# Kernel tuning notes

Hardware: AMD Instinct MI355X
Metric: run time of the kernel (lower is better)

## Reference

```python
import jax, jax.numpy as jnp
import numpy as np

D_MODEL = 768
N_HEADS = 12
HEAD_DIM = D_MODEL // N_HEADS


def setup_inputs() -> dict:
    key = jax.random.key(0)
    ks = jax.random.split(key, 9)
    B, S = 2, 2048
    x = jax.random.normal(ks[0], (B, S, D_MODEL), dtype=jnp.float32)
    s = 1.0 / np.sqrt(D_MODEL)
    Wq = jax.random.normal(ks[1], (D_MODEL, D_MODEL), dtype=jnp.float32) * s
    bq = jax.random.normal(ks[2], (D_MODEL,), dtype=jnp.float32) * 0.01
    Wk = jax.random.normal(ks[3], (D_MODEL, D_MODEL), dtype=jnp.float32) * s
    bk = jax.random.normal(ks[4], (D_MODEL,), dtype=jnp.float32) * 0.01
    Wv = jax.random.normal(ks[5], (D_MODEL, D_MODEL), dtype=jnp.float32) * s
    bv = jax.random.normal(ks[6], (D_MODEL,), dtype=jnp.float32) * 0.01
    Wo = jax.random.normal(ks[7], (D_MODEL, D_MODEL), dtype=jnp.float32) * s
    bo = jax.random.normal(ks[8], (D_MODEL,), dtype=jnp.float32) * 0.01
    return {"x": x, "Wq": Wq, "bq": bq, "Wk": Wk, "bk": bk,
            "Wv": Wv, "bv": bv, "Wo": Wo, "bo": bo}


def reference(x, Wq, bq, Wk, bk, Wv, bv, Wo, bo):
    B, S, _ = x.shape
    H, Dh = N_HEADS, HEAD_DIM
    # Projections (torch Linear: x @ W.T + b; here W stored as [in, out])
    q = (x @ Wq + bq).reshape(B, S, H, Dh)
    k = (x @ Wk + bk).reshape(B, S, H, Dh)
    v = (x @ Wv + bv).reshape(B, S, H, Dh)
    scale = 1.0 / jnp.sqrt(jnp.float32(Dh))
    # NOTE: source applies no causal mask despite the class name.
    scores = jnp.einsum('bqhd,bkhd->bhqk', q, k) * scale
    attn = jax.nn.softmax(scores, axis=-1)
    out = jnp.einsum('bhqk,bkhd->bqhd', attn, v).reshape(B, S, H * Dh)
    return out @ Wo + bo
```

## Files before the change

kernel.cpp:

```cpp
#include <hip/hip_runtime.h>

typedef unsigned short u16;
typedef __fp16 halfx8 __attribute__((ext_vector_type(8)));
typedef float floatx4 __attribute__((ext_vector_type(4)));
typedef unsigned short u16x4 __attribute__((ext_vector_type(4)));

#define D_MODEL 768
#define NH 12
#define DH 64
#define SEQ 2048
#define BATCH 2
#define MTOK 4096
#define DQKV 2304

__device__ __forceinline__ u16 f2h(float f) {
    __fp16 h = (__fp16)f;
    return __builtin_bit_cast(u16, h);
}

__device__ __forceinline__ void gload_lds16(const void* g, void* l) {
    __builtin_amdgcn_global_load_lds(
        (const __attribute__((address_space(1))) void*)g,
        (__attribute__((address_space(3))) void*)l, 16, 0, 0);
}


__global__ __launch_bounds__(256) void cvt_x_kernel(const float* __restrict__ x, u16* __restrict__ xh) {
    int i = (blockIdx.x * 256 + threadIdx.x) * 4;
    float4 v = *(const float4*)(x + i);
    u16x4 p;
    p[0] = f2h(v.x); p[1] = f2h(v.y); p[2] = f2h(v.z); p[3] = f2h(v.w);
    *(u16x4*)(xh + i) = p;
}

__global__ __launch_bounds__(256) void concat_bias_kernel(const float* __restrict__ bq, const float* __restrict__ bk,
                                                          const float* __restrict__ bv, float* __restrict__ bqkv) {
    int i = blockIdx.x * 256 + threadIdx.x;
    float v = (i < 768) ? bq[i] : (i < 1536) ? bk[i - 768] : bv[i - 1536];
    bqkv[i] = v;
}

__global__ __launch_bounds__(256) void transpose_w_kernel(const float* __restrict__ Wq, const float* __restrict__ Wk,
                                                          const float* __restrict__ Wv, const float* __restrict__ Wo,
                                                          u16* __restrict__ WqkvT, u16* __restrict__ WoT) {
    int z = blockIdx.z;
    const float* W = (z == 0) ? Wq : (z == 1) ? Wk : (z == 2) ? Wv : Wo;
    u16* dst = (z < 3) ? (WqkvT + (size_t)z * 768 * 768) : WoT;
    int k0 = blockIdx.x * 64, n0 = blockIdx.y * 64;
    __shared__ u16 t[64][72];
    int tid = threadIdx.x;
#pragma unroll
    for (int p = 0; p < 16; ++p) {
        int idx = p * 256 + tid;
        int kr = idx >> 6, nc = idx & 63;
        t[kr][nc] = f2h(W[(size_t)(k0 + kr) * 768 + n0 + nc]);
    }
    __syncthreads();
#pragma unroll
    for (int p = 0; p < 16; ++p) {
        int idx = p * 256 + tid;
        int nr = idx >> 6, kc = idx & 63;
        dst[(size_t)(n0 + nr) * 768 + k0 + kc] = t[kc][nr];
    }
}

__global__ __launch_bounds__(256) void transpose_v_kernel(const u16* __restrict__ Cqkv, u16* __restrict__ vT) {
    int st = blockIdx.x;
    int bh = blockIdx.y;
    int b = bh / NH, h = bh % NH;
    __shared__ u16 t[64][72];
    int tid = threadIdx.x;
#pragma unroll
    for (int p = 0; p < 16; ++p) {
        int idx = p * 256 + tid;
        int sl = idx >> 6, d = idx & 63;
        t[sl][d] = Cqkv[(size_t)(b * SEQ + st * 64 + sl) * DQKV + 1536 + h * DH + d];
    }
    __syncthreads();
#pragma unroll
    for (int p = 0; p < 16; ++p) {
        int idx = p * 256 + tid;
        int dl = idx >> 6, sl = idx & 63;
        vT[(size_t)(bh * 64 + dl) * SEQ + st * 64 + sl] = t[sl][dl];
    }
}


template <bool OUT_F16>
__global__ __launch_bounds__(256) void gemm_bt(const u16* __restrict__ A, const u16* __restrict__ Bt,
                                               const float* __restrict__ bias, void* __restrict__ Cout,
                                               int M, int N, int K) {
    const int tid = threadIdx.x;
    const int wid = tid >> 6;
    const int lane = tid & 63;
    const int qd = lane >> 4;
    const int l15 = lane & 15;

    const int tn = blockIdx.x * 128;
    const int tm = blockIdx.y * 128;
    const int wm = (wid >> 1) * 64;
    const int wn = (wid & 1) * 64;

    __shared__ alignas(16) u16 As[128 * 32];
    __shared__ alignas(16) u16 Bs[128 * 32];

    floatx4 acc[4][4];
#pragma unroll
    for (int i = 0; i < 4; ++i)
#pragma unroll
        for (int j = 0; j < 4; ++j) acc[i][j] = (floatx4)(0.0f);

    const u16* Arow[2];
    const u16* Brow[2];
    u16* lA[2];
    u16* lB[2];
#pragma unroll
    for (int rd = 0; rd < 2; ++rd) {
        int s = rd * 256 + wid * 64 + lane;
        int dr = s >> 3, bs = s & 7, bl = bs ^ (dr & 7);
        int r = dr * 2 + (bl >> 2), c = bl & 3;
        Arow[rd] = A + (size_t)(tm + r) * K + c * 8;
        Brow[rd] = Bt + (size_t)(tn + r) * K + c * 8;
        lA[rd] = As + (size_t)(rd * 256 + wid * 64) * 8;
        lB[rd] = Bs + (size_t)(rd * 256 + wid * 64) * 8;
    }

    for (int kb = 0; kb < K; kb += 32) {
        __syncthreads();
#pragma unroll
        for (int rd = 0; rd < 2; ++rd) {
            gload_lds16(Arow[rd] + kb, lA[rd]);
            gload_lds16(Brow[rd] + kb, lB[rd]);
        }
        __syncthreads();

        halfx8 af[4], bf[4];
#pragma unroll
        for (int i = 0; i < 4; ++i) {
            int r = wm + i * 16 + l15;
            int dr = r >> 1;
            int blk = ((r & 1) * 4 + qd) ^ (dr & 7);
            af[i] = *(const halfx8*)(As + dr * 64 + blk * 8);
            int r2 = wn + i * 16 + l15;
            int dr2 = r2 >> 1;
            int blk2 = ((r2 & 1) * 4 + qd) ^ (dr2 & 7);
            bf[i] = *(const halfx8*)(Bs + dr2 * 64 + blk2 * 8);
        }
#pragma unroll
        for (int i = 0; i < 4; ++i)
#pragma unroll
            for (int j = 0; j < 4; ++j)
                acc[i][j] = __builtin_amdgcn_mfma_f32_16x16x32_f16(af[i], bf[j], acc[i][j], 0, 0, 0);
    }

#pragma unroll
    for (int j = 0; j < 4; ++j) {
        int col = tn + wn + j * 16 + l15;
        float bv = bias[col];
#pragma unroll
        for (int i = 0; i < 4; ++i) {
            int row0 = tm + wm + i * 16 + qd * 4;
#pragma unroll
            for (int r = 0; r < 4; ++r) {
                float v = acc[i][j][r] + bv;
                if (OUT_F16)
                    ((u16*)Cout)[(size_t)(row0 + r) * N + col] = f2h(v);
                else
                    ((float*)Cout)[(size_t)(row0 + r) * N + col] = v;
            }
        }
    }
}


__global__ __launch_bounds__(256) void attn_kernel(const u16* __restrict__ Cqkv, const u16* __restrict__ vT,
                                                   u16* __restrict__ attn) {
    const int tid = threadIdx.x;
    const int wid = tid >> 6;
    const int lane = tid & 63;
    const int qd = lane >> 4;
    const int l15 = lane & 15;

    const int bh = blockIdx.y;
    const int b = bh / NH, h = bh % NH;
    const int q0 = blockIdx.x * 128;
    const int rowbase = b * SEQ + q0 + wid * 32;

    __shared__ alignas(16) u16 Ks[128 * 64];
    __shared__ alignas(16) u16 Vts[64 * 128];
    __shared__ alignas(16) u16 Ps[4][32 * 128];

    halfx8 aq[2][2];
#pragma unroll
    for (int i = 0; i < 2; ++i)
#pragma unroll
        for (int ks = 0; ks < 2; ++ks)
            aq[i][ks] = *(const halfx8*)(Cqkv + (size_t)(rowbase + i * 16 + l15) * DQKV + h * DH + ks * 32 + qd * 8);

    floatx4 o[4][2];
#pragma unroll
    for (int i = 0; i < 4; ++i)
#pragma unroll
        for (int j = 0; j < 2; ++j) o[i][j] = (floatx4)(0.0f);

    float mstate[2] = {-3.0e38f, -3.0e38f};
    float lstate[2] = {0.0f, 0.0f};
    const float cscale = 0.125f * 1.44269504088896340736f;

    u16* ps = &Ps[wid][0];

    for (int kt = 0; kt < 16; ++kt) {
        __syncthreads();
#pragma unroll
        for (int c4 = 0; c4 < 4; ++c4) {
            int s = c4 * 256 + wid * 64 + lane;
            {
                int r = s >> 3, bs = s & 7, bl = bs ^ (r & 7);
                const u16* g = Cqkv + (size_t)(b * SEQ + kt * 128 + r) * DQKV + 768 + h * DH + bl * 8;
                gload_lds16(g, Ks + (size_t)(c4 * 256 + wid * 64) * 8);
            }
            {
                int r = s >> 4, bs = s & 15, bl = bs ^ (r & 15);
                const u16* g = vT + (size_t)(bh * 64 + r) * SEQ + kt * 128 + bl * 8;
                gload_lds16(g, Vts + (size_t)(c4 * 256 + wid * 64) * 8);
            }
        }
        __syncthreads();

        floatx4 sc[8][2];
#pragma unroll
        for (int mi = 0; mi < 8; ++mi)
#pragma unroll
            for (int j2 = 0; j2 < 2; ++j2) sc[mi][j2] = (floatx4)(0.0f);
#pragma unroll
        for (int ks = 0; ks < 2; ++ks)
#pragma unroll
            for (int mi = 0; mi < 8; ++mi) {
                int r = mi * 16 + l15;
                halfx8 ak = *(const halfx8*)(Ks + r * 64 + (((ks * 4 + qd) ^ (r & 7)) * 8));
#pragma unroll
                for (int j2 = 0; j2 < 2; ++j2)
                    sc[mi][j2] = __builtin_amdgcn_mfma_f32_16x16x32_f16(ak, aq[j2][ks], sc[mi][j2], 0, 0, 0);
            }

        float mnew[2], alpha[2], rsum[2];
#pragma unroll
        for (int j2 = 0; j2 < 2; ++j2) {
            float rm = sc[0][j2][0];
#pragma unroll
            for (int mi = 0; mi < 8; ++mi)
#pragma unroll
                for (int r = 0; r < 4; ++r) rm = fmaxf(rm, sc[mi][j2][r]);
            rm = fmaxf(rm, __shfl_xor(rm, 16, 64));
            rm = fmaxf(rm, __shfl_xor(rm, 32, 64));
            mnew[j2] = fmaxf(mstate[j2], rm * cscale);
            alpha[j2] = __builtin_amdgcn_exp2f(mstate[j2] - mnew[j2]);
            mstate[j2] = mnew[j2];
            rsum[j2] = 0.0f;
        }
#pragma unroll
        for (int mi = 0; mi < 8; ++mi)
#pragma unroll
            for (int j2 = 0; j2 < 2; ++j2) {
                u16x4 pk;
#pragma unroll
                for (int r = 0; r < 4; ++r) {
                    float p = __builtin_amdgcn_exp2f(sc[mi][j2][r] * cscale - mnew[j2]);
                    rsum[j2] += p;
                    pk[r] = f2h(p);
                }
                int key0 = mi * 16 + qd * 4;
                int addr = (j2 * 16 + l15) * 128 + (((key0 >> 3) ^ l15) * 8) + (key0 & 7);
                *(u16x4*)(ps + addr) = pk;
            }
#pragma unroll
        for (int j2 = 0; j2 < 2; ++j2) {
            float s2 = rsum[j2];
            s2 += __shfl_xor(s2, 16, 64);
            s2 += __shfl_xor(s2, 32, 64);
            lstate[j2] = lstate[j2] * alpha[j2] + s2;
        }
#pragma unroll
        for (int ip = 0; ip < 4; ++ip)
#pragma unroll
            for (int j2 = 0; j2 < 2; ++j2)
#pragma unroll
                for (int r = 0; r < 4; ++r) o[ip][j2][r] *= alpha[j2];

#pragma unroll
        for (int ks2 = 0; ks2 < 4; ++ks2) {
            halfx8 bp[2];
#pragma unroll
            for (int j2 = 0; j2 < 2; ++j2)
                bp[j2] = *(const halfx8*)(ps + (j2 * 16 + l15) * 128 + (((ks2 * 4 + qd) ^ l15) * 8));
#pragma unroll
            for (int ip = 0; ip < 4; ++ip) {
                int r = ip * 16 + l15;
                halfx8 av = *(const halfx8*)(Vts + r * 128 + (((ks2 * 4 + qd) ^ (r & 15)) * 8));
#pragma unroll
                for (int j2 = 0; j2 < 2; ++j2)
                    o[ip][j2] = __builtin_amdgcn_mfma_f32_16x16x32_f16(av, bp[j2], o[ip][j2], 0, 0, 0);
            }
        }
    }

#pragma unroll
    for (int j2 = 0; j2 < 2; ++j2) {
        float inv = __builtin_amdgcn_rcpf(lstate[j2]);
        int token = rowbase + j2 * 16 + l15;
#pragma unroll
        for (int ip = 0; ip < 4; ++ip) {
            u16x4 pk;
#pragma unroll
            for (int r = 0; r < 4; ++r) pk[r] = f2h(o[ip][j2][r] * inv);
            *(u16x4*)(attn + (size_t)token * D_MODEL + h * DH + ip * 16 + qd * 4) = pk;
        }
    }
}


extern "C" void kernel_launch(void* const* d_in, const int* in_sizes, int n_in,
                              void* d_out, int out_size, void* d_ws, size_t ws_size,
                              hipStream_t stream) {
    const float* x  = (const float*)d_in[0];
    const float* Wq = (const float*)d_in[1];
    const float* bq = (const float*)d_in[2];
    const float* Wk = (const float*)d_in[3];
    const float* bk = (const float*)d_in[4];
    const float* Wv = (const float*)d_in[5];
    const float* bv = (const float*)d_in[6];
    const float* Wo = (const float*)d_in[7];
    const float* bo = (const float*)d_in[8];

    char* ws = (char*)d_ws;
    size_t off = 0;
    auto take = [&](size_t bytes) -> char* {
        char* p = ws + off;
        off += (bytes + 255) & ~(size_t)255;
        return p;
    };
    u16*   xh    = (u16*)take((size_t)MTOK * D_MODEL * 2);
    u16*   WqkvT = (u16*)take((size_t)DQKV * D_MODEL * 2);
    u16*   WoT   = (u16*)take((size_t)D_MODEL * D_MODEL * 2);
    float* bqkv  = (float*)take((size_t)DQKV * 4);
    u16*   Cqkv  = (u16*)take((size_t)MTOK * DQKV * 2);
    u16*   vTb   = (u16*)take((size_t)BATCH * NH * DH * SEQ * 2);
    u16*   attn  = (u16*)take((size_t)MTOK * D_MODEL * 2);

    cvt_x_kernel<<<MTOK * D_MODEL / 1024, 256, 0, stream>>>(x, xh);
    concat_bias_kernel<<<DQKV / 256, 256, 0, stream>>>(bq, bk, bv, bqkv);
    transpose_w_kernel<<<dim3(12, 12, 4), 256, 0, stream>>>(Wq, Wk, Wv, Wo, WqkvT, WoT);
    gemm_bt<true><<<dim3(DQKV / 128, MTOK / 128), 256, 0, stream>>>(xh, WqkvT, bqkv, Cqkv, MTOK, DQKV, D_MODEL);
    transpose_v_kernel<<<dim3(SEQ / 64, BATCH * NH), 256, 0, stream>>>(Cqkv, vTb);
    attn_kernel<<<dim3(SEQ / 128, BATCH * NH), 256, 0, stream>>>(Cqkv, vTb, attn);
    gemm_bt<false><<<dim3(D_MODEL / 128, MTOK / 128), 256, 0, stream>>>(attn, WoT, bo, d_out, MTOK, D_MODEL, D_MODEL);
}
```

Before: 201.8 us.

## Fuse prep kernels, deepen GEMM K tile, split attention keys across waves

Merges the x conversion, weight transpose and bias concat into one launch to cut launch overhead. The GEMM now stages 64-wide K tiles per barrier pair, halving the number of synchronisations. Attention now processes 64 queries per block, with each wave handling a 32-key slice of every 128-key tile; the four partial softmax states are then merged through shared memory. This doubles the grid and shrinks per-wave P storage, at the cost of a serial cross-wave merge and more accumulator registers.

```diff
diff --git a/kernel.cpp b/kernel.cpp
--- a/kernel.cpp
+++ b/kernel.cpp
@@ -4,6 +4,7 @@
 typedef __fp16 halfx8 __attribute__((ext_vector_type(8)));
 typedef float floatx4 __attribute__((ext_vector_type(4)));
 typedef unsigned short u16x4 __attribute__((ext_vector_type(4)));
+typedef unsigned short u16x8 __attribute__((ext_vector_type(8)));
 
 #define D_MODEL 768
 #define NH 12
@@ -25,42 +26,46 @@
 }
 
 
-__global__ __launch_bounds__(256) void cvt_x_kernel(const float* __restrict__ x, u16* __restrict__ xh) {
-    int i = (blockIdx.x * 256 + threadIdx.x) * 4;
-    float4 v = *(const float4*)(x + i);
-    u16x4 p;
-    p[0] = f2h(v.x); p[1] = f2h(v.y); p[2] = f2h(v.z); p[3] = f2h(v.w);
-    *(u16x4*)(xh + i) = p;
-}
-
-__global__ __launch_bounds__(256) void concat_bias_kernel(const float* __restrict__ bq, const float* __restrict__ bk,
-                                                          const float* __restrict__ bv, float* __restrict__ bqkv) {
-    int i = blockIdx.x * 256 + threadIdx.x;
-    float v = (i < 768) ? bq[i] : (i < 1536) ? bk[i - 768] : bv[i - 1536];
-    bqkv[i] = v;
-}
-
-__global__ __launch_bounds__(256) void transpose_w_kernel(const float* __restrict__ Wq, const float* __restrict__ Wk,
-                                                          const float* __restrict__ Wv, const float* __restrict__ Wo,
-                                                          u16* __restrict__ WqkvT, u16* __restrict__ WoT) {
-    int z = blockIdx.z;
-    const float* W = (z == 0) ? Wq : (z == 1) ? Wk : (z == 2) ? Wv : Wo;
-    u16* dst = (z < 3) ? (WqkvT + (size_t)z * 768 * 768) : WoT;
-    int k0 = blockIdx.x * 64, n0 = blockIdx.y * 64;
+__global__ __launch_bounds__(256) void prep_kernel(const float* __restrict__ x,
+                                                   const float* __restrict__ Wq, const float* __restrict__ Wk,
+                                                   const float* __restrict__ Wv, const float* __restrict__ Wo,
+                                                   const float* __restrict__ bq, const float* __restrict__ bk,
+                                                   const float* __restrict__ bv,
+                                                   u16* __restrict__ xh, u16* __restrict__ WqkvT,
+                                                   u16* __restrict__ WoT, float* __restrict__ bqkv) {
     __shared__ u16 t[64][72];
+    int bid = blockIdx.x;
     int tid = threadIdx.x;
-#pragma unroll
-    for (int p = 0; p < 16; ++p) {
-        int idx = p * 256 + tid;
-        int kr = idx >> 6, nc = idx & 63;
-        t[kr][nc] = f2h(W[(size_t)(k0 + kr) * 768 + n0 + nc]);
-    }
-    __syncthreads();
-#pragma unroll
-    for (int p = 0; p < 16; ++p) {
-        int idx = p * 256 + tid;
-        int nr = idx >> 6, kc = idx & 63;
-        dst[(size_t)(n0 + nr) * 768 + k0 + kc] = t[kc][nr];
+    if (bid < 3072) {
+        int i = (bid * 256 + tid) * 4;
+        float4 v = *(const float4*)(x + i);
+        u16x4 p;
+        p[0] = f2h(v.x); p[1] = f2h(v.y); p[2] = f2h(v.z); p[3] = f2h(v.w);
+        *(u16x4*)(xh + i) = p;
+    } else if (bid < 3648) {
+        int z2 = bid - 3072;
+        int z = z2 / 144;
+        int t2 = z2 % 144;
+        int k0 = (t2 / 12) * 64, n0 = (t2 % 12) * 64;
+        const float* W = (z == 0) ? Wq : (z == 1) ? Wk : (z == 2) ? Wv : Wo;
+        u16* dst = (z < 3) ? (WqkvT + (size_t)z * 768 * 768) : WoT;
+#pragma unroll
+        for (int p = 0; p < 16; ++p) {
+            int idx = p * 256 + tid;
+            int kr = idx >> 6, nc = idx & 63;
+            t[kr][nc] = f2h(W[(size_t)(k0 + kr) * 768 + n0 + nc]);
+        }
+        __syncthreads();
+#pragma unroll
+        for (int p = 0; p < 16; ++p) {
+            int idx = p * 256 + tid;
+            int nr = idx >> 6, kc = idx & 63;
+            dst[(size_t)(n0 + nr) * 768 + k0 + kc] = t[kc][nr];
+        }
+    } else {
+        int i = (bid - 3648) * 256 + tid;
+        float v = (i < 768) ? bq[i] : (i < 1536) ? bk[i - 768] : bv[i - 1536];
+        bqkv[i] = v;
     }
 }
 
@@ -101,8 +106,8 @@
     const int wm = (wid >> 1) * 64;
     const int wn = (wid & 1) * 64;
 
-    __shared__ alignas(16) u16 As[128 * 32];
-    __shared__ alignas(16) u16 Bs[128 * 32];
+    __shared__ alignas(16) u16 As[128 * 64];
+    __shared__ alignas(16) u16 Bs[128 * 64];
 
     floatx4 acc[4][4];
 #pragma unroll
@@ -110,47 +115,45 @@
 #pragma unroll
         for (int j = 0; j < 4; ++j) acc[i][j] = (floatx4)(0.0f);
 
-    const u16* Arow[2];
-    const u16* Brow[2];
-    u16* lA[2];
-    u16* lB[2];
-#pragma unroll
-    for (int rd = 0; rd < 2; ++rd) {
+    const u16* Ag[4];
+    const u16* Bg[4];
+    u16* lA[4];
+    u16* lB[4];
+#pragma unroll
+    for (int rd = 0; rd < 4; ++rd) {
         int s = rd * 256 + wid * 64 + lane;
-        int dr = s >> 3, bs = s & 7, bl = bs ^ (dr & 7);
-        int r = dr * 2 + (bl >> 2), c = bl & 3;
-        Arow[rd] = A + (size_t)(tm + r) * K + c * 8;
-        Brow[rd] = Bt + (size_t)(tn + r) * K + c * 8;
+        int r = s >> 3, bs = s & 7, bl = bs ^ (r & 7);
+        Ag[rd] = A + (size_t)(tm + r) * K + bl * 8;
+        Bg[rd] = Bt + (size_t)(tn + r) * K + bl * 8;
         lA[rd] = As + (size_t)(rd * 256 + wid * 64) * 8;
         lB[rd] = Bs + (size_t)(rd * 256 + wid * 64) * 8;
     }
 
-    for (int kb = 0; kb < K; kb += 32) {
-        __syncthreads();
-#pragma unroll
-        for (int rd = 0; rd < 2; ++rd) {
-            gload_lds16(Arow[rd] + kb, lA[rd]);
-            gload_lds16(Brow[rd] + kb, lB[rd]);
-        }
-        __syncthreads();
-
-        halfx8 af[4], bf[4];
-#pragma unroll
-        for (int i = 0; i < 4; ++i) {
-            int r = wm + i * 16 + l15;
-            int dr = r >> 1;
-            int blk = ((r & 1) * 4 + qd) ^ (dr & 7);
-            af[i] = *(const halfx8*)(As + dr * 64 + blk * 8);
-            int r2 = wn + i * 16 + l15;
-            int dr2 = r2 >> 1;
-            int blk2 = ((r2 & 1) * 4 + qd) ^ (dr2 & 7);
-            bf[i] = *(const halfx8*)(Bs + dr2 * 64 + blk2 * 8);
-        }
-#pragma unroll
-        for (int i = 0; i < 4; ++i)
-#pragma unroll
-            for (int j = 0; j < 4; ++j)
-                acc[i][j] = __builtin_amdgcn_mfma_f32_16x16x32_f16(af[i], bf[j], acc[i][j], 0, 0, 0);
+    for (int kb = 0; kb < K; kb += 64) {
+        __syncthreads();
+#pragma unroll
+        for (int rd = 0; rd < 4; ++rd) {
+            gload_lds16(Ag[rd] + kb, lA[rd]);
+            gload_lds16(Bg[rd] + kb, lB[rd]);
+        }
+        __syncthreads();
+
+#pragma unroll
+        for (int ks = 0; ks < 2; ++ks) {
+            halfx8 af[4], bf[4];
+#pragma unroll
+            for (int i = 0; i < 4; ++i) {
+                int r = wm + i * 16 + l15;
+                af[i] = *(const halfx8*)(As + r * 64 + (((ks * 4 + qd) ^ (r & 7)) * 8));
+                int r2 = wn + i * 16 + l15;
+                bf[i] = *(const halfx8*)(Bs + r2 * 64 + (((ks * 4 + qd) ^ (r2 & 7)) * 8));
+            }
+#pragma unroll
+            for (int i = 0; i < 4; ++i)
+#pragma unroll
+                for (int j = 0; j < 4; ++j)
+                    acc[i][j] = __builtin_amdgcn_mfma_f32_16x16x32_f16(af[i], bf[j], acc[i][j], 0, 0, 0);
+        }
     }
 
 #pragma unroll
@@ -173,8 +176,8 @@
 }
 
 
-__global__ __launch_bounds__(256) void attn_kernel(const u16* __restrict__ Cqkv, const u16* __restrict__ vT,
-                                                   u16* __restrict__ attn) {
+__global__ __launch_bounds__(256, 3) void attn_kernel(const u16* __restrict__ Cqkv, const u16* __restrict__ vT,
+                                                      u16* __restrict__ attn) {
     const int tid = threadIdx.x;
     const int wid = tid >> 6;
     const int lane = tid & 63;
@@ -183,31 +186,29 @@
 
     const int bh = blockIdx.y;
     const int b = bh / NH, h = bh % NH;
-    const int q0 = blockIdx.x * 128;
-    const int rowbase = b * SEQ + q0 + wid * 32;
-
-    __shared__ alignas(16) u16 Ks[128 * 64];
-    __shared__ alignas(16) u16 Vts[64 * 128];
-    __shared__ alignas(16) u16 Ps[4][32 * 128];
-
-    halfx8 aq[2][2];
-#pragma unroll
-    for (int i = 0; i < 2; ++i)
+    const int q0 = blockIdx.x * 64;
+
+    __shared__ alignas(16) u16 smem[26624];
+    u16* Ks = smem;
+    u16* Vts = smem + 8192;
+    u16* ps = smem + 16384 + wid * 2560;
+
+    halfx8 aq[4][2];
+#pragma unroll
+    for (int jn = 0; jn < 4; ++jn)
 #pragma unroll
         for (int ks = 0; ks < 2; ++ks)
-            aq[i][ks] = *(const halfx8*)(Cqkv + (size_t)(rowbase + i * 16 + l15) * DQKV + h * DH + ks * 32 + qd * 8);
-
-    floatx4 o[4][2];
-#pragma unroll
-    for (int i = 0; i < 4; ++i)
-#pragma unroll
-        for (int j = 0; j < 2; ++j) o[i][j] = (floatx4)(0.0f);
-
-    float mstate[2] = {-3.0e38f, -3.0e38f};
-    float lstate[2] = {0.0f, 0.0f};
+            aq[jn][ks] = *(const halfx8*)(Cqkv + (size_t)(b * SEQ + q0 + jn * 16 + l15) * DQKV + h * DH + ks * 32 + qd * 8);
+
+    floatx4 o[4][4];
+#pragma unroll
+    for (int ip = 0; ip < 4; ++ip)
+#pragma unroll
+        for (int jn = 0; jn < 4; ++jn) o[ip][jn] = (floatx4)(0.0f);
+
+    float mstate[4] = {-3.0e38f, -3.0e38f, -3.0e38f, -3.0e38f};
+    float lstate[4] = {0.0f, 0.0f, 0.0f, 0.0f};
     const float cscale = 0.125f * 1.44269504088896340736f;
-
-    u16* ps = &Ps[wid][0];
 
     for (int kt = 0; kt < 16; ++kt) {
         __syncthreads();
@@ -216,105 +217,137 @@
             int s = c4 * 256 + wid * 64 + lane;
             {
                 int r = s >> 3, bs = s & 7, bl = bs ^ (r & 7);
-                const u16* g = Cqkv + (size_t)(b * SEQ + kt * 128 + r) * DQKV + 768 + h * DH + bl * 8;
-                gload_lds16(g, Ks + (size_t)(c4 * 256 + wid * 64) * 8);
+                gload_lds16(Cqkv + (size_t)(b * SEQ + kt * 128 + r) * DQKV + 768 + h * DH + bl * 8,
+                            Ks + (size_t)(c4 * 256 + wid * 64) * 8);
             }
             {
                 int r = s >> 4, bs = s & 15, bl = bs ^ (r & 15);
-                const u16* g = vT + (size_t)(bh * 64 + r) * SEQ + kt * 128 + bl * 8;
-                gload_lds16(g, Vts + (size_t)(c4 * 256 + wid * 64) * 8);
-            }
-        }
-        __syncthreads();
-
-        floatx4 sc[8][2];
-#pragma unroll
-        for (int mi = 0; mi < 8; ++mi)
-#pragma unroll
-            for (int j2 = 0; j2 < 2; ++j2) sc[mi][j2] = (floatx4)(0.0f);
+                gload_lds16(vT + (size_t)(bh * 64 + r) * SEQ + kt * 128 + bl * 8,
+                            Vts + (size_t)(c4 * 256 + wid * 64) * 8);
+            }
+        }
+        __syncthreads();
+
+        floatx4 sc[2][4];
+#pragma unroll
+        for (int mi = 0; mi < 2; ++mi)
+#pragma unroll
+            for (int jn = 0; jn < 4; ++jn) sc[mi][jn] = (floatx4)(0.0f);
 #pragma unroll
         for (int ks = 0; ks < 2; ++ks)
 #pragma unroll
-            for (int mi = 0; mi < 8; ++mi) {
-                int r = mi * 16 + l15;
+            for (int mi = 0; mi < 2; ++mi) {
+                int r = wid * 32 + mi * 16 + l15;
                 halfx8 ak = *(const halfx8*)(Ks + r * 64 + (((ks * 4 + qd) ^ (r & 7)) * 8));
 #pragma unroll
-                for (int j2 = 0; j2 < 2; ++j2)
-                    sc[mi][j2] = __builtin_amdgcn_mfma_f32_16x16x32_f16(ak, aq[j2][ks], sc[mi][j2], 0, 0, 0);
-            }
-
-        float mnew[2], alpha[2], rsum[2];
-#pragma unroll
-        for (int j2 = 0; j2 < 2; ++j2) {
-            float rm = sc[0][j2][0];
-#pragma unroll
-            for (int mi = 0; mi < 8; ++mi)
-#pragma unroll
-                for (int r = 0; r < 4; ++r) rm = fmaxf(rm, sc[mi][j2][r]);
+                for (int jn = 0; jn < 4; ++jn)
+                    sc[mi][jn] = __builtin_amdgcn_mfma_f32_16x16x32_f16(ak, aq[jn][ks], sc[mi][jn], 0, 0, 0);
+            }
+
+        float mnew[4], alpha[4], rsum[4];
+#pragma unroll
+        for (int jn = 0; jn < 4; ++jn) {
+            float rm = sc[0][jn][0];
+#pragma unroll
+            for (int mi = 0; mi < 2; ++mi)
+#pragma unroll
+                for (int r = 0; r < 4; ++r) rm = fmaxf(rm, sc[mi][jn][r]);
             rm = fmaxf(rm, __shfl_xor(rm, 16, 64));
             rm = fmaxf(rm, __shfl_xor(rm, 32, 64));
-            mnew[j2] = fmaxf(mstate[j2], rm * cscale);
-            alpha[j2] = __builtin_amdgcn_exp2f(mstate[j2] - mnew[j2]);
-            mstate[j2] = mnew[j2];
-            rsum[j2] = 0.0f;
-        }
-#pragma unroll
-        for (int mi = 0; mi < 8; ++mi)
-#pragma unroll
-            for (int j2 = 0; j2 < 2; ++j2) {
+            mnew[jn] = fmaxf(mstate[jn], rm * cscale);
+            alpha[jn] = __builtin_amdgcn_exp2f(mstate[jn] - mnew[jn]);
+            mstate[jn] = mnew[jn];
+            rsum[jn] = 0.0f;
+        }
+#pragma unroll
+        for (int mi = 0; mi < 2; ++mi)
+#pragma unroll
+            for (int jn = 0; jn < 4; ++jn) {
                 u16x4 pk;
 #pragma unroll
                 for (int r = 0; r < 4; ++r) {
-                    float p = __builtin_amdgcn_exp2f(sc[mi][j2][r] * cscale - mnew[j2]);
-                    rsum[j2] += p;
+                    float p = __builtin_amdgcn_exp2f(sc[mi][jn][r] * cscale - mnew[jn]);
+                    rsum[jn] += p;
                     pk[r] = f2h(p);
                 }
                 int key0 = mi * 16 + qd * 4;
-                int addr = (j2 * 16 + l15) * 128 + (((key0 >> 3) ^ l15) * 8) + (key0 & 7);
-                *(u16x4*)(ps + addr) = pk;
-            }
-#pragma unroll
-        for (int j2 = 0; j2 < 2; ++j2) {
-            float s2 = rsum[j2];
+                *(u16x4*)(ps + (jn * 16 + l15) * 40 + key0) = pk;
+            }
+#pragma unroll
+        for (int jn = 0; jn < 4; ++jn) {
+            float s2 = rsum[jn];
             s2 += __shfl_xor(s2, 16, 64);
             s2 += __shfl_xor(s2, 32, 64);
-            lstate[j2] = lstate[j2] * alpha[j2] + s2;
-        }
-#pragma unroll
-        for (int ip = 0; ip < 4; ++ip)
-#pragma unroll
-            for (int j2 = 0; j2 < 2; ++j2)
-#pragma unroll
-                for (int r = 0; r < 4; ++r) o[ip][j2][r] *= alpha[j2];
-
-#pragma unroll
-        for (int ks2 = 0; ks2 < 4; ++ks2) {
-            halfx8 bp[2];
-#pragma unroll
-            for (int j2 = 0; j2 < 2; ++j2)
-                bp[j2] = *(const halfx8*)(ps + (j2 * 16 + l15) * 128 + (((ks2 * 4 + qd) ^ l15) * 8));
-#pragma unroll
-            for (int ip = 0; ip < 4; ++ip) {
-                int r = ip * 16 + l15;
-                halfx8 av = *(const halfx8*)(Vts + r * 128 + (((ks2 * 4 + qd) ^ (r & 15)) * 8));
-#pragma unroll
-                for (int j2 = 0; j2 < 2; ++j2)
-                    o[ip][j2] = __builtin_amdgcn_mfma_f32_16x16x32_f16(av, bp[j2], o[ip][j2], 0, 0, 0);
-            }
-        }
-    }
-
-#pragma unroll
-    for (int j2 = 0; j2 < 2; ++j2) {
-        float inv = __builtin_amdgcn_rcpf(lstate[j2]);
-        int token = rowbase + j2 * 16 + l15;
+            lstate[jn] = lstate[jn] * alpha[jn] + s2;
+#pragma unroll
+            for (int ip = 0; ip < 4; ++ip)
+#pragma unroll
+                for (int r = 0; r < 4; ++r) o[ip][jn][r] *= alpha[jn];
+        }
+
+        halfx8 bp[4];
+#pragma unroll
+        for (int jn = 0; jn < 4; ++jn)
+            bp[jn] = *(const halfx8*)(ps + (jn * 16 + l15) * 40 + qd * 8);
 #pragma unroll
         for (int ip = 0; ip < 4; ++ip) {
-            u16x4 pk;
-#pragma unroll
-            for (int r = 0; r < 4; ++r) pk[r] = f2h(o[ip][j2][r] * inv);
-            *(u16x4*)(attn + (size_t)token * D_MODEL + h * DH + ip * 16 + qd * 4) = pk;
-        }
+            int r = ip * 16 + l15;
+            halfx8 av = *(const halfx8*)(Vts + r * 128 + (((wid * 4 + qd) ^ (r & 15)) * 8));
+#pragma unroll
+            for (int jn = 0; jn < 4; ++jn)
+                o[ip][jn] = __builtin_amdgcn_mfma_f32_16x16x32_f16(av, bp[jn], o[ip][jn], 0, 0, 0);
+        }
+    }
+
+    float* Oacc = (float*)smem;
+    float* ma = (float*)smem + 4352;
+    float* la = ma + 64;
+
+    __syncthreads();
+    if (wid == 0) {
+#pragma unroll
+        for (int jn = 0; jn < 4; ++jn) {
+            int q = jn * 16 + l15;
+#pragma unroll
+            for (int ip = 0; ip < 4; ++ip)
+                *(floatx4*)(Oacc + q * 68 + ip * 16 + qd * 4) = o[ip][jn];
+            if (qd == 0) { ma[q] = mstate[jn]; la[q] = lstate[jn]; }
+        }
+    }
+    for (int w = 1; w < 4; ++w) {
+        __syncthreads();
+        if (wid == w) {
+#pragma unroll
+            for (int jn = 0; jn < 4; ++jn) {
+                int q = jn * 16 + l15;
+                float mo = ma[q], lo = la[q];
+                float mstar = fmaxf(mo, mstate[jn]);
+                float fo = __builtin_amdgcn_exp2f(mo - mstar);
+                float fw = __builtin_amdgcn_exp2f(mstate[jn] - mstar);
+#pragma unroll
+                for (int ip = 0; ip < 4; ++ip) {
+                    float* p = Oacc + q * 68 + ip * 16 + qd * 4;
+                    floatx4 prev = *(floatx4*)p;
+                    *(floatx4*)p = prev * fo + o[ip][jn] * fw;
+                }
+                if (qd == 0) { ma[q] = mstar; la[q] = lo * fo + lstate[jn] * fw; }
+            }
+        }
+    }
+    __syncthreads();
+
+    {
+        int q = tid >> 2, d0 = (tid & 3) * 16;
+        float inv = __builtin_amdgcn_rcpf(la[q]);
+        const float* op = Oacc + q * 68 + d0;
+        u16x8 pk0, pk1;
+#pragma unroll
+        for (int r = 0; r < 8; ++r) pk0[r] = f2h(op[r] * inv);
+#pragma unroll
+        for (int r = 0; r < 8; ++r) pk1[r] = f2h(op[8 + r] * inv);
+        u16* dst = attn + (size_t)(b * SEQ + q0 + q) * D_MODEL + h * DH + d0;
+        *(u16x8*)dst = pk0;
+        *(u16x8*)(dst + 8) = pk1;
     }
 }
 
@@ -347,11 +380,9 @@
     u16*   vTb   = (u16*)take((size_t)BATCH * NH * DH * SEQ * 2);
     u16*   attn  = (u16*)take((size_t)MTOK * D_MODEL * 2);
 
-    cvt_x_kernel<<<MTOK * D_MODEL / 1024, 256, 0, stream>>>(x, xh);
-    concat_bias_kernel<<<DQKV / 256, 256, 0, stream>>>(bq, bk, bv, bqkv);
-    transpose_w_kernel<<<dim3(12, 12, 4), 256, 0, stream>>>(Wq, Wk, Wv, Wo, WqkvT, WoT);
+    prep_kernel<<<3657, 256, 0, stream>>>(x, Wq, Wk, Wv, Wo, bq, bk, bv, xh, WqkvT, WoT, bqkv);
     gemm_bt<true><<<dim3(DQKV / 128, MTOK / 128), 256, 0, stream>>>(xh, WqkvT, bqkv, Cqkv, MTOK, DQKV, D_MODEL);
     transpose_v_kernel<<<dim3(SEQ / 64, BATCH * NH), 256, 0, stream>>>(Cqkv, vTb);
-    attn_kernel<<<dim3(SEQ / 128, BATCH * NH), 256, 0, stream>>>(Cqkv, vTb, attn);
+    attn_kernel<<<dim3(SEQ / 64, BATCH * NH), 256, 0, stream>>>(Cqkv, vTb, attn);
     gemm_bt<false><<<dim3(D_MODEL / 128, MTOK / 128), 256, 0, stream>>>(attn, WoT, bo, d_out, MTOK, D_MODEL, D_MODEL);
 }
```

Measured after the change: 209.6 us. 3.9% more time.
